# Kernel optimization log

Hardware: AMD Instinct MI355X
Metric: run time of the kernel (lower is better)

The kernel has to match this reference:

```python
import jax, jax.numpy as jnp
import numpy as np

N_BINS = 15


def setup_inputs() -> dict:
    key = jax.random.key(0)
    k1, k2 = jax.random.split(key)
    N, C = 2000000, 64
    probabilities = jax.random.uniform(k1, (N, C), dtype=jnp.float32)
    labels = jax.random.randint(k2, (N,), 0, C, dtype=jnp.int64)
    return {"probabilities": probabilities, "labels": labels}


def reference(probabilities, labels):
    # confidences/predictions over class dim
    confidences = jnp.max(probabilities, axis=1)
    predictions = jnp.argmax(probabilities, axis=1)
    accuracies = (predictions == labels).astype(confidences.dtype)

    boundaries = jnp.linspace(0.0, 1.0, N_BINS + 1)
    # torch loop uses (lower, upper] bins; digitize(right=True) gives index i
    # s.t. boundaries[i-1] < x <= boundaries[i]. conf == 0 falls in no bin.
    bin_idx = jnp.clip(jnp.digitize(confidences, boundaries, right=True) - 1, 0, N_BINS - 1)
    valid = (confidences > 0).astype(confidences.dtype)

    sum_conf = jax.ops.segment_sum(confidences * valid, bin_idx, num_segments=N_BINS)
    sum_acc = jax.ops.segment_sum(accuracies * valid, bin_idx, num_segments=N_BINS)
    count = jax.ops.segment_sum(valid, bin_idx, num_segments=N_BINS)

    n = confidences.shape[0]
    prop_in_bin = count / n
    safe = jnp.maximum(count, 1.0)
    avg_conf = sum_conf / safe
    avg_acc = sum_acc / safe
    per_bin = jnp.where(count > 0, jnp.abs(avg_conf - avg_acc) * prop_in_bin, 0.0)
    ece = jnp.sum(per_bin)
    return ece.reshape(1)
```

## Files before the change

kernel.cpp:

```cpp
#include <hip/hip_runtime.h>
#include <hip/hip_bf16.h>

#define N_BINS 15
#define C_DIM 64


__global__ __launch_bounds__(256) void ece_main(const float* __restrict__ probs,
                                                const int* __restrict__ labels,
                                                float* __restrict__ gbins, int N) {
    __shared__ float s_bins[3 * N_BINS];
    const int tid = threadIdx.x;
    if (tid < 3 * N_BINS) s_bins[tid] = 0.f;
    __syncthreads();

    float c14 = 0.f, a14 = 0.f, n14 = 0.f;
    float c13 = 0.f, a13 = 0.f, n13 = 0.f;

    const int stride = gridDim.x * blockDim.x;
    for (int row = blockIdx.x * blockDim.x + tid; row < N; row += stride) {
        const int lab = labels[row];
        const float4* p4 = (const float4*)(probs + (size_t)row * C_DIM);

        float4 v[16];
        #pragma unroll
        for (int j = 0; j < 16; j++) v[j] = p4[j];

        float best = v[0].x; int idx = 0;
        #pragma unroll
        for (int j = 0; j < 16; j++) {
            if (v[j].x > best) { best = v[j].x; idx = 4 * j + 0; }
            if (v[j].y > best) { best = v[j].y; idx = 4 * j + 1; }
            if (v[j].z > best) { best = v[j].z; idx = 4 * j + 2; }
            if (v[j].w > best) { best = v[j].w; idx = 4 * j + 3; }
        }

        const float conf = best;
        const float acc = (idx == lab) ? 1.f : 0.f;
        if (conf > 0.f) {
            int bin = (int)ceilf(conf * 15.f) - 1;
            bin = min(max(bin, 0), N_BINS - 1);
            if (bin == 14)      { c14 += conf; a14 += acc; n14 += 1.f; }
            else if (bin == 13) { c13 += conf; a13 += acc; n13 += 1.f; }
            else {
                atomicAdd(&s_bins[bin],             conf);
                atomicAdd(&s_bins[N_BINS + bin],    acc);
                atomicAdd(&s_bins[2 * N_BINS + bin], 1.f);
            }
        }
    }

    #pragma unroll
    for (int off = 32; off > 0; off >>= 1) {
        c14 += __shfl_xor(c14, off, 64);
        a14 += __shfl_xor(a14, off, 64);
        n14 += __shfl_xor(n14, off, 64);
        c13 += __shfl_xor(c13, off, 64);
        a13 += __shfl_xor(a13, off, 64);
        n13 += __shfl_xor(n13, off, 64);
    }
    if ((tid & 63) == 0) {
        atomicAdd(&s_bins[14],              c14);
        atomicAdd(&s_bins[N_BINS + 14],     a14);
        atomicAdd(&s_bins[2 * N_BINS + 14], n14);
        atomicAdd(&s_bins[13],              c13);
        atomicAdd(&s_bins[N_BINS + 13],     a13);
        atomicAdd(&s_bins[2 * N_BINS + 13], n13);
    }
    __syncthreads();
    if (tid < 3 * N_BINS) atomicAdd(&gbins[tid], s_bins[tid]);
}

__global__ void ece_final(const float* __restrict__ gbins,
                          float* __restrict__ out, int N) {
    if (threadIdx.x == 0 && blockIdx.x == 0) {
        float ece = 0.f;
        const float invN = 1.f / (float)N;
        for (int b = 0; b < N_BINS; b++) {
            const float sc = gbins[b];
            const float sa = gbins[N_BINS + b];
            const float cn = gbins[2 * N_BINS + b];
            if (cn > 0.f) {
                const float avg_conf = sc / cn;
                const float avg_acc  = sa / cn;
                ece += fabsf(avg_conf - avg_acc) * (cn * invN);
            }
        }
        out[0] = ece;
    }
}

extern "C" void kernel_launch(void* const* d_in, const int* in_sizes, int n_in,
                              void* d_out, int out_size, void* d_ws, size_t ws_size,
                              hipStream_t stream) {
    const float* probs  = (const float*)d_in[0];
    const int*   labels = (const int*)d_in[1];
    float* gbins = (float*)d_ws;
    float* out   = (float*)d_out;

    const int N = in_sizes[1];

    hipMemsetAsync(d_ws, 0, 3 * N_BINS * sizeof(float), stream);

    const int threads = 256;
    const int blocks  = 2048;
    ece_main<<<blocks, threads, 0, stream>>>(probs, labels, gbins, N);
    ece_final<<<1, 64, 0, stream>>>(gbins, out, N);
}
```

Measured before the change: 667.0 us.

## Coalesce row loads by splitting each row across 16 lanes with shuffle argmax

Each row is now read by 16 lanes, each loading one float4, so a wave reads 4 contiguous rows per load and every access is coalesced. Before, each thread strided through its own 256-byte row. Per-row max and argmax are found with a 4-step xor-shuffle reduction that breaks ties toward the lower index, and one lane per row does the binning. Each wave handles 4 groups of 4 rows per iteration to keep several loads in flight. This adds shuffle work and leaves 15 of 16 lanes idle during binning, in exchange for better memory access efficiency. Global atomics for zero-valued bins are also skipped.

Result: no change. 662.6 us (-0.7%).

```diff
diff --git a/kernel.cpp b/kernel.cpp
--- a/kernel.cpp
+++ b/kernel.cpp
@@ -13,44 +13,83 @@
     if (tid < 3 * N_BINS) s_bins[tid] = 0.f;
     __syncthreads();
 
+    const int lane = tid & 63;
+    const int wave = tid >> 6;
+    const int sub  = lane >> 4;
+    const int l16  = lane & 15;
+    const int wavesPerBlock = blockDim.x >> 6;
+
     float c14 = 0.f, a14 = 0.f, n14 = 0.f;
     float c13 = 0.f, a13 = 0.f, n13 = 0.f;
 
-    const int stride = gridDim.x * blockDim.x;
-    for (int row = blockIdx.x * blockDim.x + tid; row < N; row += stride) {
-        const int lab = labels[row];
-        const float4* p4 = (const float4*)(probs + (size_t)row * C_DIM);
+    const long long nGroups = ((long long)N + 3) >> 2;
+    long long g0 = ((long long)blockIdx.x * wavesPerBlock + wave) * 4;
+    const long long gstride = (long long)gridDim.x * wavesPerBlock * 4;
 
-        float4 v[16];
-        #pragma unroll
-        for (int j = 0; j < 16; j++) v[j] = p4[j];
+    for (; g0 < nGroups; g0 += gstride) {
+        float4 v[4];
+        int lab[4];
+        bool rv[4];
 
-        float best = v[0].x; int idx = 0;
-        #pragma unroll
-        for (int j = 0; j < 16; j++) {
-            if (v[j].x > best) { best = v[j].x; idx = 4 * j + 0; }
-            if (v[j].y > best) { best = v[j].y; idx = 4 * j + 1; }
-            if (v[j].z > best) { best = v[j].z; idx = 4 * j + 2; }
-            if (v[j].w > best) { best = v[j].w; idx = 4 * j + 3; }
+        const bool fullIter = (g0 * 4 + 16) <= (long long)N;
+        if (fullIter) {
+            #pragma unroll
+            for (int gi = 0; gi < 4; gi++) {
+                const long long grp = g0 + gi;
+                v[gi] = *(const float4*)(probs + grp * 256 + lane * 4);
+                rv[gi] = true;
+                if (l16 == 0) lab[gi] = labels[grp * 4 + sub];
+            }
+        } else {
+            #pragma unroll
+            for (int gi = 0; gi < 4; gi++) {
+                const long long grp = g0 + gi;
+                const long long row = grp * 4 + sub;
+                rv[gi] = (grp < nGroups) && (row < (long long)N);
+                if (rv[gi]) {
+                    v[gi] = *(const float4*)(probs + grp * 256 + lane * 4);
+                    if (l16 == 0) lab[gi] = labels[row];
+                } else {
+                    v[gi] = make_float4(-1.f, -1.f, -1.f, -1.f);
+                }
+            }
         }
 
-        const float conf = best;
-        const float acc = (idx == lab) ? 1.f : 0.f;
-        if (conf > 0.f) {
-            int bin = (int)ceilf(conf * 15.f) - 1;
-            bin = min(max(bin, 0), N_BINS - 1);
-            if (bin == 14)      { c14 += conf; a14 += acc; n14 += 1.f; }
-            else if (bin == 13) { c13 += conf; a13 += acc; n13 += 1.f; }
-            else {
-                atomicAdd(&s_bins[bin],             conf);
-                atomicAdd(&s_bins[N_BINS + bin],    acc);
-                atomicAdd(&s_bins[2 * N_BINS + bin], 1.f);
+        #pragma unroll
+        for (int gi = 0; gi < 4; gi++) {
+            float conf; int pred;
+            {
+                const float4 x = v[gi];
+                float m = x.x; int a = l16 * 4;
+                if (x.y > m) { m = x.y; a = l16 * 4 + 1; }
+                if (x.z > m) { m = x.z; a = l16 * 4 + 2; }
+                if (x.w > m) { m = x.w; a = l16 * 4 + 3; }
+                conf = rv[gi] ? m : -1.f;
+                pred = a;
+            }
+            #pragma unroll
+            for (int off = 1; off < 16; off <<= 1) {
+                const float om = __shfl_xor(conf, off, 64);
+                const int   oa = __shfl_xor(pred, off, 64);
+                if (om > conf || (om == conf && oa < pred)) { conf = om; pred = oa; }
+            }
+            if (l16 == 0 && rv[gi] && conf > 0.f) {
+                const float acc = (pred == lab[gi]) ? 1.f : 0.f;
+                int bin = (int)ceilf(conf * 15.f) - 1;
+                bin = min(max(bin, 0), N_BINS - 1);
+                if (bin == 14)      { c14 += conf; a14 += acc; n14 += 1.f; }
+                else if (bin == 13) { c13 += conf; a13 += acc; n13 += 1.f; }
+                else {
+                    atomicAdd(&s_bins[bin],              conf);
+                    atomicAdd(&s_bins[N_BINS + bin],     acc);
+                    atomicAdd(&s_bins[2 * N_BINS + bin], 1.f);
+                }
             }
         }
     }
 
     #pragma unroll
-    for (int off = 32; off > 0; off >>= 1) {
+    for (int off = 16; off <= 32; off <<= 1) {
         c14 += __shfl_xor(c14, off, 64);
         a14 += __shfl_xor(a14, off, 64);
         n14 += __shfl_xor(n14, off, 64);
@@ -58,7 +97,7 @@
         a13 += __shfl_xor(a13, off, 64);
         n13 += __shfl_xor(n13, off, 64);
     }
-    if ((tid & 63) == 0) {
+    if (lane == 0) {
         atomicAdd(&s_bins[14],              c14);
         atomicAdd(&s_bins[N_BINS + 14],     a14);
         atomicAdd(&s_bins[2 * N_BINS + 14], n14);
@@ -67,7 +106,7 @@
         atomicAdd(&s_bins[2 * N_BINS + 13], n13);
     }
     __syncthreads();
-    if (tid < 3 * N_BINS) atomicAdd(&gbins[tid], s_bins[tid]);
+    if (tid < 3 * N_BINS && s_bins[tid] != 0.f) atomicAdd(&gbins[tid], s_bins[tid]);
 }
 
 __global__ void ece_final(const float* __restrict__ gbins,
```
